# Kernel tuning notes

Hardware: AMD Instinct MI355X
Metric: run time of the kernel (lower is better)

The kernel has to match this reference:

```python
import jax, jax.numpy as jnp
import numpy as np

EPS = 1e-5

def layer_norm(x, g, b):
    mu = jnp.mean(x, axis=-1, keepdims=True)
    var = jnp.mean(jnp.square(x - mu), axis=-1, keepdims=True)
    return (x - mu) * jax.lax.rsqrt(var + EPS) * g + b

def setup_inputs() -> dict:
    B, T, C, H = 8, 1024, 1024, 16
    hs = C // H
    key = jax.random.key(0)
    ks = jax.random.split(key, 12)
    s = 0.02
    return {
        "x": jax.random.normal(ks[0], (B, T, C), dtype=jnp.float32),
        # per-head projections, stacked: [H, C, hs]
        "wq": jax.random.normal(ks[1], (H, C, hs), dtype=jnp.float32) * s,
        "wk": jax.random.normal(ks[2], (H, C, hs), dtype=jnp.float32) * s,
        "wv": jax.random.normal(ks[3], (H, C, hs), dtype=jnp.float32) * s,
        "w_proj": jax.random.normal(ks[4], (C, C), dtype=jnp.float32) * s,
        "b_proj": jnp.zeros((C,), dtype=jnp.float32),
        "ln1_g": jnp.ones((C,), dtype=jnp.float32),
        "ln1_b": jnp.zeros((C,), dtype=jnp.float32),
        "ln2_g": jnp.ones((C,), dtype=jnp.float32),
        "ln2_b": jnp.zeros((C,), dtype=jnp.float32),
        "w1": jax.random.normal(ks[5], (C, 4 * C), dtype=jnp.float32) * s,
        "b1": jnp.zeros((4 * C,), dtype=jnp.float32),
        "w2": jax.random.normal(ks[6], (4 * C, C), dtype=jnp.float32) * s,
        "b2": jnp.zeros((C,), dtype=jnp.float32),
    }

def reference(x, wq, wk, wv, w_proj, b_proj, ln1_g, ln1_b, ln2_g, ln2_b, w1, b1, w2, b2):
    B, T, C = x.shape
    # --- self-attention (pre-norm) ---
    h = layer_norm(x, ln1_g, ln1_b)                      # [B,T,C]
    q = jnp.einsum('btc,hcd->bhtd', h, wq)               # [B,H,T,hs]
    k = jnp.einsum('btc,hcd->bhtd', h, wk)
    v = jnp.einsum('btc,hcd->bhtd', h, wv)
    # NOTE: original scales by C**-0.5 with C = n_embed (not head_size)
    scores = jnp.einsum('bhtd,bhsd->bhts', q, k) * (C ** -0.5)
    causal = jnp.tril(jnp.ones((T, T), dtype=bool))
    scores = jnp.where(causal, scores, -jnp.inf)
    att = jax.nn.softmax(scores, axis=-1)                # dropout is identity (eval)
    out = jnp.einsum('bhts,bhsd->bhtd', att, v)          # [B,H,T,hs]
    out = out.transpose(0, 2, 1, 3).reshape(B, T, C)     # concat heads
    x = x + out @ w_proj + b_proj
    # --- feed-forward (pre-norm) ---
    h2 = layer_norm(x, ln2_g, ln2_b)
    x = x + jax.nn.relu(h2 @ w1 + b1) @ w2 + b2
    return x
```

## Files before the change

### kernel.cpp

```cpp
#include <hip/hip_runtime.h>
#include <cstdint>

typedef __attribute__((ext_vector_type(8))) __bf16 bf16x8;
typedef __attribute__((ext_vector_type(4))) float f32x4;

__device__ __forceinline__ unsigned short f2bf(float f) {
  union { float f; unsigned int u; } v; v.f = f;
  unsigned int u = v.u;
  return (unsigned short)((u + 0x7FFFu + ((u >> 16) & 1u)) >> 16);
}

__device__ __forceinline__ void load_lds16(const unsigned short* g, unsigned short* l) {
  __builtin_amdgcn_global_load_lds(
      (const __attribute__((address_space(1))) unsigned int*)g,
      (__attribute__((address_space(3))) unsigned int*)l, 16, 0, 0);
}

__global__ void transpose_all(const float* __restrict__ wq, const float* __restrict__ wk,
                              const float* __restrict__ wv, const float* __restrict__ w_proj,
                              const float* __restrict__ w1, const float* __restrict__ w2,
                              unsigned short* __restrict__ qkvt, unsigned short* __restrict__ projt,
                              unsigned short* __restrict__ w1t, unsigned short* __restrict__ w2t) {
  __shared__ float tile[32][33];
  const int id = blockIdx.x;
  const float* src;
  unsigned short* dst;
  int K, N, nt, kt;
  if (id < 3072) {
    const int which = id >> 10, rem = id & 1023;
    const int slice = rem >> 6, t = rem & 63;
    src = (which == 0 ? wq : which == 1 ? wk : wv) + (long)slice * 65536;
    dst = qkvt + (long)which * 1048576 + (long)slice * 65536;
    K = 1024; N = 64;
    nt = (t & 1) * 32; kt = (t >> 1) * 32;
  } else if (id < 4096) {
    const int t = id - 3072;
    src = w_proj; dst = projt; K = 1024; N = 1024;
    nt = (t & 31) * 32; kt = (t >> 5) * 32;
  } else if (id < 8192) {
    const int t = id - 4096;
    src = w1; dst = w1t; K = 1024; N = 4096;
    nt = (t & 127) * 32; kt = (t >> 7) * 32;
  } else {
    const int t = id - 8192;
    src = w2; dst = w2t; K = 4096; N = 1024;
    nt = (t & 31) * 32; kt = (t >> 5) * 32;
  }
  const int tx = threadIdx.x & 31, ty = threadIdx.x >> 5;
#pragma unroll
  for (int i = 0; i < 4; i++)
    tile[ty + 8 * i][tx] = src[(long)(kt + ty + 8 * i) * N + nt + tx];
  __syncthreads();
#pragma unroll
  for (int i = 0; i < 4; i++)
    dst[(long)(nt + ty + 8 * i) * K + kt + tx] = f2bf(tile[tx][ty + 8 * i]);
}

__global__ __launch_bounds__(256, 4) void ln_kernel(const float* __restrict__ x,
                                                    const float* __restrict__ g,
                                                    const float* __restrict__ b,
                                                    unsigned short* __restrict__ out) {
  const int row = blockIdx.x, tid = threadIdx.x;
  const int wave = tid >> 6, lane = tid & 63;
  const float4 xv = *(const float4*)&x[(long)row * 1024 + tid * 4];
  float s1 = xv.x + xv.y + xv.z + xv.w;
  float s2 = xv.x * xv.x + xv.y * xv.y + xv.z * xv.z + xv.w * xv.w;
#pragma unroll
  for (int m = 1; m < 64; m <<= 1) { s1 += __shfl_xor(s1, m); s2 += __shfl_xor(s2, m); }
  __shared__ float a1[4], a2[4];
  if (lane == 0) { a1[wave] = s1; a2[wave] = s2; }
  __syncthreads();
  s1 = a1[0] + a1[1] + a1[2] + a1[3];
  s2 = a2[0] + a2[1] + a2[2] + a2[3];
  const float mu = s1 * (1.f / 1024.f);
  const float var = s2 * (1.f / 1024.f) - mu * mu;
  const float rs = rsqrtf(var + 1e-5f);
  const float4 gv = *(const float4*)&g[tid * 4];
  const float4 bv = *(const float4*)&b[tid * 4];
  ushort4 o;
  o.x = f2bf((xv.x - mu) * rs * gv.x + bv.x);
  o.y = f2bf((xv.y - mu) * rs * gv.y + bv.y);
  o.z = f2bf((xv.z - mu) * rs * gv.z + bv.z);
  o.w = f2bf((xv.w - mu) * rs * gv.w + bv.w);
  *(ushort4*)&out[(long)row * 1024 + tid * 4] = o;
}

#define EPI_QKV 0
#define EPI_F32 1
#define EPI_RELU 2

template <int EPI>
__global__ __launch_bounds__(256, 3) void gemm_bt(
    const unsigned short* __restrict__ A, const unsigned short* __restrict__ Bt,
    int M, int N, int K,
    const float* __restrict__ bias, const float* __restrict__ resid,
    float* __restrict__ outF, unsigned short* __restrict__ outB,
    unsigned short* __restrict__ qb, unsigned short* __restrict__ kb,
    unsigned short* __restrict__ vTb) {
  __shared__ __attribute__((aligned(16))) unsigned short Alds[128 * 64];
  __shared__ __attribute__((aligned(16))) unsigned short Blds[128 * 64];
  const int tid = threadIdx.x;
  const int wave = tid >> 6, lane = tid & 63;
  const int quad = lane >> 4, l15 = lane & 15;
  const long tM = (long)blockIdx.x * 128;
  const long tN = (long)blockIdx.y * 128;
  const int wm = (wave >> 1) * 64, wn = (wave & 1) * 64;

  const unsigned short* aP[4];
  const unsigned short* bP[4];
  unsigned short* lA[4];
  unsigned short* lB[4];
#pragma unroll
  for (int qq = 0; qq < 4; qq++) {
    int p = (qq * 4 + wave) * 64 + lane;
    int m = p >> 3;
    int kc = (p & 7) ^ (m & 7);
    aP[qq] = A + (tM + m) * K + kc * 8;
    bP[qq] = Bt + (tN + m) * K + kc * 8;
    lA[qq] = Alds + (qq * 4 + wave) * 512;
    lB[qq] = Blds + (qq * 4 + wave) * 512;
  }

  f32x4 acc[4][4];
#pragma unroll
  for (int i = 0; i < 4; i++)
#pragma unroll
    for (int j = 0; j < 4; j++) acc[i][j] = (f32x4){0.f, 0.f, 0.f, 0.f};

  for (int k0 = 0; k0 < K; k0 += 64) {
    __syncthreads();
#pragma unroll
    for (int qq = 0; qq < 4; qq++) {
      load_lds16(aP[qq], lA[qq]);
      load_lds16(bP[qq], lB[qq]);
      aP[qq] += 64;
      bP[qq] += 64;
    }
    __syncthreads();
#pragma unroll
    for (int ks = 0; ks < 2; ks++) {
      bf16x8 af[4], bfr[4];
#pragma unroll
      for (int mt = 0; mt < 4; mt++) {
        int ml = wm + mt * 16 + l15;
        int pc = (ks * 4 + quad) ^ (ml & 7);
        af[mt] = *(const bf16x8*)&Alds[(ml * 8 + pc) * 8];
      }
#pragma unroll
      for (int nt = 0; nt < 4; nt++) {
        int nl = wn + nt * 16 + l15;
        int pc = (ks * 4 + quad) ^ (nl & 7);
        bfr[nt] = *(const bf16x8*)&Blds[(nl * 8 + pc) * 8];
      }
#pragma unroll
      for (int mt = 0; mt < 4; mt++)
#pragma unroll
        for (int nt = 0; nt < 4; nt++)
          acc[mt][nt] = __builtin_amdgcn_mfma_f32_16x16x32_bf16(af[mt], bfr[nt], acc[mt][nt], 0, 0, 0);
    }
  }

#pragma unroll
  for (int mt = 0; mt < 4; mt++) {
#pragma unroll
    for (int nt = 0; nt < 4; nt++) {
      const long col = tN + wn + nt * 16 + l15;
      const long row0 = tM + wm + mt * 16 + quad * 4;
      if (EPI == EPI_F32) {
        const float bv = bias[col];
#pragma unroll
        for (int r = 0; r < 4; r++) {
          long idx = (row0 + r) * N + col;
          outF[idx] = acc[mt][nt][r] + bv + resid[idx];
        }
      } else if (EPI == EPI_RELU) {
        const float bv = bias[col];
#pragma unroll
        for (int r = 0; r < 4; r++) {
          float v = acc[mt][nt][r] + bv;
          outB[(row0 + r) * N + col] = f2bf(v > 0.f ? v : 0.f);
        }
      } else {
        const int which = (int)(col >> 10);
        const int hh = (int)((col >> 6) & 15);
        const int dd = (int)(col & 63);
        const int b = (int)(row0 >> 10), t0 = (int)(row0 & 1023);
        if (which == 2) {
          ushort4 pk;
          pk.x = f2bf(acc[mt][nt][0]);
          pk.y = f2bf(acc[mt][nt][1]);
          pk.z = f2bf(acc[mt][nt][2]);
          pk.w = f2bf(acc[mt][nt][3]);
          *(ushort4*)&vTb[(long)(b * 16 + hh) * 65536 + dd * 1024 + t0] = pk;
        } else {
          unsigned short* dst = (which == 0 ? qb : kb);
#pragma unroll
          for (int r = 0; r < 4; r++)
            dst[((b * 16 + hh) * 1024 + t0 + r) * 64 + dd] = f2bf(acc[mt][nt][r]);
        }
      }
    }
  }
}

__global__ __launch_bounds__(256, 4) void attn_kernel(const unsigned short* __restrict__ qb,
                                                      const unsigned short* __restrict__ kb,
                                                      const unsigned short* __restrict__ vTb,
                                                      unsigned short* __restrict__ out) {
  __shared__ __attribute__((aligned(16))) unsigned short Klds[64 * 64];
  __shared__ __attribute__((aligned(16))) unsigned short Vlds[64 * 64];
  __shared__ __attribute__((aligned(16))) unsigned short Plds[4 * 16 * 68];
  const int bh = blockIdx.x;
  const int qt2 = blockIdx.y;
  const int tid = threadIdx.x;
  const int wave = tid >> 6, lane = tid & 63;
  const int quad = lane >> 4, l15 = lane & 15;

  const unsigned short* qp = qb + (long)bh * 65536;
  const unsigned short* kp = kb + (long)bh * 65536;
  const unsigned short* vp = vTb + (long)bh * 65536;

  bf16x8 qf[2][2];
#pragma unroll
  for (int g = 0; g < 2; g++) {
    const int qrow = qt2 * 128 + (wave * 2 + g) * 16 + l15;
    qf[g][0] = *(const bf16x8*)&qp[qrow * 64 + quad * 8];
    qf[g][1] = *(const bf16x8*)&qp[qrow * 64 + 32 + quad * 8];
  }

  f32x4 O[2][4];
  float l_r[2][4];
#pragma unroll
  for (int g = 0; g < 2; g++) {
#pragma unroll
    for (int nt = 0; nt < 4; nt++) O[g][nt] = (f32x4){0.f, 0.f, 0.f, 0.f};
#pragma unroll
    for (int r = 0; r < 4; r++) l_r[g][r] = 0.f;
  }

  unsigned short* Pl = Plds + wave * (16 * 68);
  const float cscale = 0.045084220f;
  const int kmax = 2 * qt2 + 1;

  for (int kt = 0; kt <= kmax; kt++) {
    __syncthreads();
#pragma unroll
    for (int c = 0; c < 2; c++) {
      const int pb = (wave * 2 + c) * 64;
      const int p = pb + lane;
      const int m = p >> 3;
      const int kc = (p & 7) ^ (m & 7);
      load_lds16(kp + (kt * 64 + m) * 64 + kc * 8, Klds + pb * 8);
      load_lds16(vp + m * 1024 + kt * 64 + kc * 8, Vlds + pb * 8);
    }
    __syncthreads();

#pragma unroll
    for (int g = 0; g < 2; g++) {
      const int rowbase = qt2 * 128 + (wave * 2 + g) * 16;
      if (kt * 64 >= rowbase + 16) continue;

      f32x4 S[4];
#pragma unroll
      for (int nt = 0; nt < 4; nt++) {
        const int row = nt * 16 + l15;
        const int pc0 = quad ^ (row & 7);
        const int pc1 = (quad + 4) ^ (row & 7);
        bf16x8 kf0 = *(const bf16x8*)&Klds[(row * 8 + pc0) * 8];
        bf16x8 kf1 = *(const bf16x8*)&Klds[(row * 8 + pc1) * 8];
        f32x4 s = (f32x4){0.f, 0.f, 0.f, 0.f};
        s = __builtin_amdgcn_mfma_f32_16x16x32_bf16(qf[g][0], kf0, s, 0, 0, 0);
        s = __builtin_amdgcn_mfma_f32_16x16x32_bf16(qf[g][1], kf1, s, 0, 0, 0);
        S[nt] = s;
      }

      const bool diag = (kt * 64 + 63 > rowbase);
      const int tb = rowbase + quad * 4;
#pragma unroll
      for (int nt = 0; nt < 4; nt++) {
        const int sg = kt * 64 + nt * 16 + l15;
#pragma unroll
        for (int r = 0; r < 4; r++) {
          float pv = exp2f(S[nt][r] * cscale);
          if (diag && sg > tb + r) pv = 0.f;
          l_r[g][r] += pv;
          Pl[(quad * 4 + r) * 68 + nt * 16 + l15] = f2bf(pv);
        }
      }
      __threadfence_block();

#pragma unroll
      for (int ks2 = 0; ks2 < 2; ks2++) {
        bf16x8 pa = *(const bf16x8*)&Pl[l15 * 68 + ks2 * 32 + quad * 8];
#pragma unroll
        for (int nt = 0; nt < 4; nt++) {
          const int d = nt * 16 + l15;
          const int pc = (ks2 * 4 + quad) ^ (d & 7);
          bf16x8 vf = *(const bf16x8*)&Vlds[(d * 8 + pc) * 8];
          O[g][nt] = __builtin_amdgcn_mfma_f32_16x16x32_bf16(pa, vf, O[g][nt], 0, 0, 0);
        }
      }
      __threadfence_block();
    }
  }

  const int b = bh >> 4, h = bh & 15;
#pragma unroll
  for (int g = 0; g < 2; g++) {
#pragma unroll
    for (int r = 0; r < 4; r++) {
      float lv = l_r[g][r];
      lv += __shfl_xor(lv, 1);
      lv += __shfl_xor(lv, 2);
      lv += __shfl_xor(lv, 4);
      lv += __shfl_xor(lv, 8);
      lv = __builtin_amdgcn_rcpf(lv);
      const int t = qt2 * 128 + (wave * 2 + g) * 16 + quad * 4 + r;
#pragma unroll
      for (int nt = 0; nt < 4; nt++)
        out[(long)(b * 1024 + t) * 1024 + h * 64 + nt * 16 + l15] = f2bf(O[g][nt][r] * lv);
    }
  }
}

extern "C" void kernel_launch(void* const* d_in, const int* in_sizes, int n_in,
                              void* d_out, int out_size, void* d_ws, size_t ws_size,
                              hipStream_t stream) {
  const float* x = (const float*)d_in[0];
  const float* wq = (const float*)d_in[1];
  const float* wk = (const float*)d_in[2];
  const float* wv = (const float*)d_in[3];
  const float* w_proj = (const float*)d_in[4];
  const float* b_proj = (const float*)d_in[5];
  const float* ln1_g = (const float*)d_in[6];
  const float* ln1_b = (const float*)d_in[7];
  const float* ln2_g = (const float*)d_in[8];
  const float* ln2_b = (const float*)d_in[9];
  const float* w1 = (const float*)d_in[10];
  const float* b1 = (const float*)d_in[11];
  const float* w2 = (const float*)d_in[12];
  const float* b2 = (const float*)d_in[13];
  float* out = (float*)d_out;

  char* w = (char*)d_ws;
  unsigned short* h1 = (unsigned short*)w;      w += (size_t)8192 * 1024 * 2;
  unsigned short* wqkvt = (unsigned short*)w;   w += (size_t)3072 * 1024 * 2;
  unsigned short* wprojt = (unsigned short*)w;  w += (size_t)1024 * 1024 * 2;
  unsigned short* w1t = (unsigned short*)w;     w += (size_t)4096 * 1024 * 2;
  unsigned short* w2t = (unsigned short*)w;     w += (size_t)4096 * 1024 * 2;
  unsigned short* qbuf = (unsigned short*)w;    w += (size_t)128 * 1024 * 64 * 2;
  unsigned short* kbuf = (unsigned short*)w;    w += (size_t)128 * 1024 * 64 * 2;
  unsigned short* vTbuf = (unsigned short*)w;   w += (size_t)128 * 1024 * 64 * 2;
  unsigned short* act = (unsigned short*)w;     w += (size_t)8192 * 4096 * 2;
  unsigned short* attnO = h1;
  unsigned short* h2 = qbuf;

  transpose_all<<<12288, 256, 0, stream>>>(wq, wk, wv, w_proj, w1, w2,
                                           wqkvt, wprojt, w1t, w2t);

  ln_kernel<<<8192, 256, 0, stream>>>(x, ln1_g, ln1_b, h1);

  gemm_bt<EPI_QKV><<<dim3(64, 24), 256, 0, stream>>>(h1, wqkvt, 8192, 3072, 1024,
                                                     nullptr, nullptr, nullptr, nullptr,
                                                     qbuf, kbuf, vTbuf);

  attn_kernel<<<dim3(128, 8), 256, 0, stream>>>(qbuf, kbuf, vTbuf, attnO);

  gemm_bt<EPI_F32><<<dim3(64, 8), 256, 0, stream>>>(attnO, wprojt, 8192, 1024, 1024,
                                                    b_proj, x, out, nullptr,
                                                    nullptr, nullptr, nullptr);

  ln_kernel<<<8192, 256, 0, stream>>>(out, ln2_g, ln2_b, h2);

  gemm_bt<EPI_RELU><<<dim3(64, 32), 256, 0, stream>>>(h2, w1t, 8192, 4096, 1024,
                                                      b1, nullptr, nullptr, act,
                                                      nullptr, nullptr, nullptr);

  gemm_bt<EPI_F32><<<dim3(64, 8), 256, 0, stream>>>(act, w2t, 8192, 1024, 4096,
                                                    b2, out, out, nullptr,
                                                    nullptr, nullptr, nullptr);
}
```

Measured before the change: 449.9 us.

## Balance causal attention work across blocks and merge LN1 into weight prep kernel

Each attention block now handles two query tiles paired as j and 7-j, so every block does the same amount of causal work, and the grid drops to 4 in y. K/V staging now loads two 64-key tiles per barrier pair into doubled LDS buffers, halving the number of syncs. Launch bounds go from 4 to 2 blocks per SM. The first layernorm is folded into the weight transpose kernel as extra blocks, which saves one launch. The risks are lower occupancy and fewer blocks in the attention grid.

```diff
diff --git a/kernel.cpp b/kernel.cpp
--- a/kernel.cpp
+++ b/kernel.cpp
@@ -16,13 +16,45 @@
       (__attribute__((address_space(3))) unsigned int*)l, 16, 0, 0);
 }
 
-__global__ void transpose_all(const float* __restrict__ wq, const float* __restrict__ wk,
-                              const float* __restrict__ wv, const float* __restrict__ w_proj,
-                              const float* __restrict__ w1, const float* __restrict__ w2,
-                              unsigned short* __restrict__ qkvt, unsigned short* __restrict__ projt,
-                              unsigned short* __restrict__ w1t, unsigned short* __restrict__ w2t) {
+__global__ void prep_kernel(const float* __restrict__ wq, const float* __restrict__ wk,
+                            const float* __restrict__ wv, const float* __restrict__ w_proj,
+                            const float* __restrict__ w1, const float* __restrict__ w2,
+                            const float* __restrict__ x, const float* __restrict__ ln1_g,
+                            const float* __restrict__ ln1_b,
+                            unsigned short* __restrict__ qkvt, unsigned short* __restrict__ projt,
+                            unsigned short* __restrict__ w1t, unsigned short* __restrict__ w2t,
+                            unsigned short* __restrict__ h1) {
   __shared__ float tile[32][33];
+  __shared__ float a1[4], a2[4];
   const int id = blockIdx.x;
+  const int tid = threadIdx.x;
+
+  if (id >= 12288) {
+    const int row = id - 12288;
+    const int wave = tid >> 6, lane = tid & 63;
+    const float4 xv = *(const float4*)&x[(long)row * 1024 + tid * 4];
+    float s1 = xv.x + xv.y + xv.z + xv.w;
+    float s2 = xv.x * xv.x + xv.y * xv.y + xv.z * xv.z + xv.w * xv.w;
+#pragma unroll
+    for (int m = 1; m < 64; m <<= 1) { s1 += __shfl_xor(s1, m); s2 += __shfl_xor(s2, m); }
+    if (lane == 0) { a1[wave] = s1; a2[wave] = s2; }
+    __syncthreads();
+    s1 = a1[0] + a1[1] + a1[2] + a1[3];
+    s2 = a2[0] + a2[1] + a2[2] + a2[3];
+    const float mu = s1 * (1.f / 1024.f);
+    const float var = s2 * (1.f / 1024.f) - mu * mu;
+    const float rs = rsqrtf(var + 1e-5f);
+    const float4 gv = *(const float4*)&ln1_g[tid * 4];
+    const float4 bv = *(const float4*)&ln1_b[tid * 4];
+    ushort4 o;
+    o.x = f2bf((xv.x - mu) * rs * gv.x + bv.x);
+    o.y = f2bf((xv.y - mu) * rs * gv.y + bv.y);
+    o.z = f2bf((xv.z - mu) * rs * gv.z + bv.z);
+    o.w = f2bf((xv.w - mu) * rs * gv.w + bv.w);
+    *(ushort4*)&h1[(long)row * 1024 + tid * 4] = o;
+    return;
+  }
+
   const float* src;
   unsigned short* dst;
   int K, N, nt, kt;
@@ -46,7 +78,7 @@
     src = w2; dst = w2t; K = 4096; N = 1024;
     nt = (t & 31) * 32; kt = (t >> 5) * 32;
   }
-  const int tx = threadIdx.x & 31, ty = threadIdx.x >> 5;
+  const int tx = tid & 31, ty = tid >> 5;
 #pragma unroll
   for (int i = 0; i < 4; i++)
     tile[ty + 8 * i][tx] = src[(long)(kt + ty + 8 * i) * N + nt + tx];
@@ -203,15 +235,15 @@
   }
 }
 
-__global__ __launch_bounds__(256, 4) void attn_kernel(const unsigned short* __restrict__ qb,
+__global__ __launch_bounds__(256, 2) void attn_kernel(const unsigned short* __restrict__ qb,
                                                       const unsigned short* __restrict__ kb,
                                                       const unsigned short* __restrict__ vTb,
                                                       unsigned short* __restrict__ out) {
-  __shared__ __attribute__((aligned(16))) unsigned short Klds[64 * 64];
-  __shared__ __attribute__((aligned(16))) unsigned short Vlds[64 * 64];
+  __shared__ __attribute__((aligned(16))) unsigned short Klds[2][64 * 64];
+  __shared__ __attribute__((aligned(16))) unsigned short Vlds[2][64 * 64];
   __shared__ __attribute__((aligned(16))) unsigned short Plds[4 * 16 * 68];
   const int bh = blockIdx.x;
-  const int qt2 = blockIdx.y;
+  const int j = blockIdx.y;
   const int tid = threadIdx.x;
   const int wave = tid >> 6, lane = tid & 63;
   const int quad = lane >> 4, l15 = lane & 15;
@@ -219,106 +251,120 @@
   const unsigned short* qp = qb + (long)bh * 65536;
   const unsigned short* kp = kb + (long)bh * 65536;
   const unsigned short* vp = vTb + (long)bh * 65536;
-
-  bf16x8 qf[2][2];
-#pragma unroll
-  for (int g = 0; g < 2; g++) {
-    const int qrow = qt2 * 128 + (wave * 2 + g) * 16 + l15;
-    qf[g][0] = *(const bf16x8*)&qp[qrow * 64 + quad * 8];
-    qf[g][1] = *(const bf16x8*)&qp[qrow * 64 + 32 + quad * 8];
-  }
-
-  f32x4 O[2][4];
-  float l_r[2][4];
-#pragma unroll
-  for (int g = 0; g < 2; g++) {
-#pragma unroll
-    for (int nt = 0; nt < 4; nt++) O[g][nt] = (f32x4){0.f, 0.f, 0.f, 0.f};
-#pragma unroll
-    for (int r = 0; r < 4; r++) l_r[g][r] = 0.f;
-  }
+  const int b = bh >> 4, h = bh & 15;
 
   unsigned short* Pl = Plds + wave * (16 * 68);
   const float cscale = 0.045084220f;
-  const int kmax = 2 * qt2 + 1;
-
-  for (int kt = 0; kt <= kmax; kt++) {
-    __syncthreads();
-#pragma unroll
-    for (int c = 0; c < 2; c++) {
-      const int pb = (wave * 2 + c) * 64;
-      const int p = pb + lane;
-      const int m = p >> 3;
-      const int kc = (p & 7) ^ (m & 7);
-      load_lds16(kp + (kt * 64 + m) * 64 + kc * 8, Klds + pb * 8);
-      load_lds16(vp + m * 1024 + kt * 64 + kc * 8, Vlds + pb * 8);
-    }
-    __syncthreads();
-
+
+  for (int ph = 0; ph < 2; ph++) {
+    const int qt2 = ph ? 7 - j : j;
+
+    bf16x8 qf[2][2];
 #pragma unroll
     for (int g = 0; g < 2; g++) {
-      const int rowbase = qt2 * 128 + (wave * 2 + g) * 16;
-      if (kt * 64 >= rowbase + 16) continue;
-
-      f32x4 S[4];
-#pragma unroll
-      for (int nt = 0; nt < 4; nt++) {
-        const int row = nt * 16 + l15;
-        const int pc0 = quad ^ (row & 7);
-        const int pc1 = (quad + 4) ^ (row & 7);
-        bf16x8 kf0 = *(const bf16x8*)&Klds[(row * 8 + pc0) * 8];
-        bf16x8 kf1 = *(const bf16x8*)&Klds[(row * 8 + pc1) * 8];
-        f32x4 s = (f32x4){0.f, 0.f, 0.f, 0.f};
-        s = __builtin_amdgcn_mfma_f32_16x16x32_bf16(qf[g][0], kf0, s, 0, 0, 0);
-        s = __builtin_amdgcn_mfma_f32_16x16x32_bf16(qf[g][1], kf1, s, 0, 0, 0);
-        S[nt] = s;
-      }
-
-      const bool diag = (kt * 64 + 63 > rowbase);
-      const int tb = rowbase + quad * 4;
-#pragma unroll
-      for (int nt = 0; nt < 4; nt++) {
-        const int sg = kt * 64 + nt * 16 + l15;
-#pragma unroll
-        for (int r = 0; r < 4; r++) {
-          float pv = exp2f(S[nt][r] * cscale);
-          if (diag && sg > tb + r) pv = 0.f;
-          l_r[g][r] += pv;
-          Pl[(quad * 4 + r) * 68 + nt * 16 + l15] = f2bf(pv);
+      const int qrow = qt2 * 128 + (wave * 2 + g) * 16 + l15;
+      qf[g][0] = *(const bf16x8*)&qp[qrow * 64 + quad * 8];
+      qf[g][1] = *(const bf16x8*)&qp[qrow * 64 + 32 + quad * 8];
+    }
+
+    f32x4 O[2][4];
+    float l_r[2][4];
+#pragma unroll
+    for (int g = 0; g < 2; g++) {
+#pragma unroll
+      for (int nt = 0; nt < 4; nt++) O[g][nt] = (f32x4){0.f, 0.f, 0.f, 0.f};
+#pragma unroll
+      for (int r = 0; r < 4; r++) l_r[g][r] = 0.f;
+    }
+
+    const int nstage = qt2 + 1;
+    for (int st = 0; st < nstage; st++) {
+      __syncthreads();
+#pragma unroll
+      for (int c = 0; c < 4; c++) {
+        const int pb = c * 256 + wave * 64;
+        const int p = pb + lane;
+        const int sub = p >> 9;
+        const int q_ = p & 511;
+        const int m = q_ >> 3;
+        const int kc = (q_ & 7) ^ (m & 7);
+        const int kt = st * 2 + sub;
+        load_lds16(kp + (kt * 64 + m) * 64 + kc * 8, (unsigned short*)Klds + pb * 8);
+        load_lds16(vp + m * 1024 + kt * 64 + kc * 8, (unsigned short*)Vlds + pb * 8);
+      }
+      __syncthreads();
+
+#pragma unroll
+      for (int sub = 0; sub < 2; sub++) {
+        const int kt = st * 2 + sub;
+        const unsigned short* Ksub = (const unsigned short*)Klds + sub * 4096;
+        const unsigned short* Vsub = (const unsigned short*)Vlds + sub * 4096;
+
+#pragma unroll
+        for (int g = 0; g < 2; g++) {
+          const int rowbase = qt2 * 128 + (wave * 2 + g) * 16;
+          if (kt * 64 >= rowbase + 16) continue;
+
+          f32x4 S[4];
+#pragma unroll
+          for (int nt = 0; nt < 4; nt++) {
+            const int row = nt * 16 + l15;
+            const int pc0 = quad ^ (row & 7);
+            const int pc1 = (quad + 4) ^ (row & 7);
+            bf16x8 kf0 = *(const bf16x8*)&Ksub[(row * 8 + pc0) * 8];
+            bf16x8 kf1 = *(const bf16x8*)&Ksub[(row * 8 + pc1) * 8];
+            f32x4 s = (f32x4){0.f, 0.f, 0.f, 0.f};
+            s = __builtin_amdgcn_mfma_f32_16x16x32_bf16(qf[g][0], kf0, s, 0, 0, 0);
+            s = __builtin_amdgcn_mfma_f32_16x16x32_bf16(qf[g][1], kf1, s, 0, 0, 0);
+            S[nt] = s;
+          }
+
+          const bool diag = (kt * 64 + 63 > rowbase);
+          const int tb = rowbase + quad * 4;
+#pragma unroll
+          for (int nt = 0; nt < 4; nt++) {
+            const int sg = kt * 64 + nt * 16 + l15;
+#pragma unroll
+            for (int r = 0; r < 4; r++) {
+              float pv = exp2f(S[nt][r] * cscale);
+              if (diag && sg > tb + r) pv = 0.f;
+              l_r[g][r] += pv;
+              Pl[(quad * 4 + r) * 68 + nt * 16 + l15] = f2bf(pv);
+            }
+          }
+          __threadfence_block();
+
+#pragma unroll
+          for (int ks2 = 0; ks2 < 2; ks2++) {
+            bf16x8 pa = *(const bf16x8*)&Pl[l15 * 68 + ks2 * 32 + quad * 8];
+#pragma unroll
+            for (int nt = 0; nt < 4; nt++) {
+              const int d = nt * 16 + l15;
+              const int pc = (ks2 * 4 + quad) ^ (d & 7);
+              bf16x8 vf = *(const bf16x8*)&Vsub[(d * 8 + pc) * 8];
+              O[g][nt] = __builtin_amdgcn_mfma_f32_16x16x32_bf16(pa, vf, O[g][nt], 0, 0, 0);
+            }
+          }
+          __threadfence_block();
         }
       }
-      __threadfence_block();
-
-#pragma unroll
-      for (int ks2 = 0; ks2 < 2; ks2++) {
-        bf16x8 pa = *(const bf16x8*)&Pl[l15 * 68 + ks2 * 32 + quad * 8];
-#pragma unroll
-        for (int nt = 0; nt < 4; nt++) {
-          const int d = nt * 16 + l15;
-          const int pc = (ks2 * 4 + quad) ^ (d & 7);
-          bf16x8 vf = *(const bf16x8*)&Vlds[(d * 8 + pc) * 8];
-          O[g][nt] = __builtin_amdgcn_mfma_f32_16x16x32_bf16(pa, vf, O[g][nt], 0, 0, 0);
-        }
-      }
-      __threadfence_block();
-    }
-  }
-
-  const int b = bh >> 4, h = bh & 15;
-#pragma unroll
-  for (int g = 0; g < 2; g++) {
-#pragma unroll
-    for (int r = 0; r < 4; r++) {
-      float lv = l_r[g][r];
-      lv += __shfl_xor(lv, 1);
-      lv += __shfl_xor(lv, 2);
-      lv += __shfl_xor(lv, 4);
-      lv += __shfl_xor(lv, 8);
-      lv = __builtin_amdgcn_rcpf(lv);
-      const int t = qt2 * 128 + (wave * 2 + g) * 16 + quad * 4 + r;
-#pragma unroll
-      for (int nt = 0; nt < 4; nt++)
-        out[(long)(b * 1024 + t) * 1024 + h * 64 + nt * 16 + l15] = f2bf(O[g][nt][r] * lv);
+    }
+
+#pragma unroll
+    for (int g = 0; g < 2; g++) {
+#pragma unroll
+      for (int r = 0; r < 4; r++) {
+        float lv = l_r[g][r];
+        lv += __shfl_xor(lv, 1);
+        lv += __shfl_xor(lv, 2);
+        lv += __shfl_xor(lv, 4);
+        lv += __shfl_xor(lv, 8);
+        lv = __builtin_amdgcn_rcpf(lv);
+        const int t = qt2 * 128 + (wave * 2 + g) * 16 + quad * 4 + r;
+#pragma unroll
+        for (int nt = 0; nt < 4; nt++)
+          out[(long)(b * 1024 + t) * 1024 + h * 64 + nt * 16 + l15] = f2bf(O[g][nt][r] * lv);
+      }
     }
   }
 }
@@ -355,16 +401,15 @@
   unsigned short* attnO = h1;
   unsigned short* h2 = qbuf;
 
-  transpose_all<<<12288, 256, 0, stream>>>(wq, wk, wv, w_proj, w1, w2,
-                                           wqkvt, wprojt, w1t, w2t);
-
-  ln_kernel<<<8192, 256, 0, stream>>>(x, ln1_g, ln1_b, h1);
+  prep_kernel<<<12288 + 8192, 256, 0, stream>>>(wq, wk, wv, w_proj, w1, w2,
+                                                x, ln1_g, ln1_b,
+                                                wqkvt, wprojt, w1t, w2t, h1);
 
   gemm_bt<EPI_QKV><<<dim3(64, 24), 256, 0, stream>>>(h1, wqkvt, 8192, 3072, 1024,
                                                      nullptr, nullptr, nullptr, nullptr,
                                                      qbuf, kbuf, vTbuf);
 
-  attn_kernel<<<dim3(128, 8), 256, 0, stream>>>(qbuf, kbuf, vTbuf, attnO);
+  attn_kernel<<<dim3(128, 4), 256, 0, stream>>>(qbuf, kbuf, vTbuf, attnO);
 
   gemm_bt<EPI_F32><<<dim3(64, 8), 256, 0, stream>>>(attnO, wprojt, 8192, 1024, 1024,
                                                     b_proj, x, out, nullptr,
```

New measurement: 438.4 us. 1.03x faster.
